# Performance work log

Hardware: AMD Instinct MI355X
Metric: run time of the kernel (lower is better)

## Reference

```python
import jax, jax.numpy as jnp
import numpy as np

B, S, D, H = 1, 2048, 768, 12
HD = D // H


def layer_norm(x, g, b, eps=1e-5):
    mu = x.mean(-1, keepdims=True)
    var = ((x - mu) ** 2).mean(-1, keepdims=True)
    return (x - mu) * jax.lax.rsqrt(var + eps) * g + b


def setup_inputs() -> dict:
    key = jax.random.key(0)
    ks = jax.random.split(key, 16)
    s = 0.02
    exp_encodings = jax.random.normal(ks[0], (B, S, D), dtype=jnp.float32)
    pert_encodings = jax.random.normal(ks[1], (B, S, D), dtype=jnp.float32)
    adj = (jax.random.uniform(ks[2], (S, S)) < 0.01).astype(jnp.int32)
    adj = adj.at[jnp.arange(S), jnp.arange(S)].set(1)
    in_proj_w = jax.random.normal(ks[3], (3 * D, D)) * s
    in_proj_b = jnp.zeros((3 * D,), jnp.float32)
    out_proj_w = jax.random.normal(ks[4], (D, D)) * s
    out_proj_b = jnp.zeros((D,), jnp.float32)
    ln0_g = jnp.ones((D,), jnp.float32); ln0_b = jnp.zeros((D,), jnp.float32)
    ln1_g = jnp.ones((D,), jnp.float32); ln1_b = jnp.zeros((D,), jnp.float32)
    ln2_g = jnp.ones((D,), jnp.float32); ln2_b = jnp.zeros((D,), jnp.float32)
    w1 = jax.random.normal(ks[5], (D // 2, D)) * s
    b1 = jnp.zeros((D // 2,), jnp.float32)
    w2 = jax.random.normal(ks[6], (D, D // 2)) * s
    b2 = jnp.zeros((D,), jnp.float32)
    return dict(exp_encodings=exp_encodings, pert_encodings=pert_encodings,
                in_proj_w=in_proj_w, in_proj_b=in_proj_b,
                out_proj_w=out_proj_w, out_proj_b=out_proj_b,
                ln0_g=ln0_g, ln0_b=ln0_b, ln1_g=ln1_g, ln1_b=ln1_b,
                ln2_g=ln2_g, ln2_b=ln2_b, w1=w1, b1=b1, w2=w2, b2=b2,
                adj=adj)


def reference(exp_encodings, pert_encodings, in_proj_w, in_proj_b,
              out_proj_w, out_proj_b, ln0_g, ln0_b, ln1_g, ln1_b,
              ln2_g, ln2_b, w1, b1, w2, b2, adj):
    b, s, d = exp_encodings.shape
    hd = d // H
    # additive mask: 0 where edge, -inf elsewhere (diag guaranteed edge)
    mask = jnp.where(adj > 0, 0.0, -jnp.inf).astype(exp_encodings.dtype)
    x_in = layer_norm(exp_encodings + pert_encodings, ln0_g, ln0_b)
    # torch MultiheadAttention (batch_first) self-attention
    qkv = x_in @ in_proj_w.T + in_proj_b          # [b,s,3d]
    q, k, v = jnp.split(qkv, 3, axis=-1)
    q = q.reshape(b, s, H, hd)
    k = k.reshape(b, s, H, hd)
    v = v.reshape(b, s, H, hd)
    scores = jnp.einsum('bqhe,bkhe->bhqk', q, k) / np.sqrt(hd) + mask
    attn = jax.nn.softmax(scores, axis=-1)
    o = jnp.einsum('bhqk,bkhe->bqhe', attn, v).reshape(b, s, d)
    o = o @ out_proj_w.T + out_proj_b
    x = layer_norm(o + x_in, ln1_g, ln1_b)
    ff = jax.nn.relu(x @ w1.T + b1) @ w2.T + b2
    return layer_norm(x + ff, ln2_g, ln2_b)
```

## Files before the change

kernel.cpp:

```cpp
#include <hip/hip_runtime.h>

#define S 2048
#define D 768
#define NH 12
#define HD 64
#define TD (3 * D)

typedef __bf16 bf16_t;
typedef __bf16 v8bf __attribute__((ext_vector_type(8)));
typedef __bf16 v4bf __attribute__((ext_vector_type(4)));
typedef float v4f __attribute__((ext_vector_type(4)));

__device__ __forceinline__ float wave_reduce_sum(float v) {
#pragma unroll
    for (int o = 32; o > 0; o >>= 1) v += __shfl_down(v, o, 64);
    return v;
}
__device__ float block_reduce_sum(float v) {
    __shared__ float t4[4];
    int lane = threadIdx.x & 63, wid = threadIdx.x >> 6;
    v = wave_reduce_sum(v);
    __syncthreads();
    if (lane == 0) t4[wid] = v;
    __syncthreads();
    return t4[0] + t4[1] + t4[2] + t4[3];
}

#define NW0 (TD * D / 4)
#define NW1 (D * D / 4)
#define NW2 ((D / 2) * D / 4)
#define NW3 (D * (D / 2) / 4)
#define NWALL (NW0 + NW1 + NW2 + NW3)

__global__ __launch_bounds__(256) void addln_cvt(const float* __restrict__ A, const float* __restrict__ Bv,
                                                 const float* __restrict__ g, const float* __restrict__ be,
                                                 bf16_t* __restrict__ out,
                                                 const float* __restrict__ s0, const float* __restrict__ s1,
                                                 const float* __restrict__ s2, const float* __restrict__ s3,
                                                 bf16_t* __restrict__ d0, bf16_t* __restrict__ d1,
                                                 bf16_t* __restrict__ d2, bf16_t* __restrict__ d3) {
    int blk = blockIdx.x, t = threadIdx.x;
    if (blk >= S) {
        int i = (blk - S) * 256 + t;
        const float* sp; bf16_t* dp;
        if (i < NW0) { sp = s0; dp = d0; }
        else if (i < NW0 + NW1) { sp = s1; dp = d1; i -= NW0; }
        else if (i < NW0 + NW1 + NW2) { sp = s2; dp = d2; i -= NW0 + NW1; }
        else if (i < NWALL) { sp = s3; dp = d3; i -= NW0 + NW1 + NW2; }
        else return;
        float4 v = ((const float4*)sp)[i];
        v4bf o = {(bf16_t)v.x, (bf16_t)v.y, (bf16_t)v.z, (bf16_t)v.w};
        *(v4bf*)(dp + (size_t)i * 4) = o;
        return;
    }
    int row = blk;
    const float* a = A + (size_t)row * D;
    const float* b = Bv + (size_t)row * D;
    float x[3];
    float s = 0.f;
#pragma unroll
    for (int i = 0; i < 3; ++i) { int c = t + 256 * i; x[i] = a[c] + b[c]; s += x[i]; }
    float mean = block_reduce_sum(s) * (1.0f / D);
    float vs = 0.f;
#pragma unroll
    for (int i = 0; i < 3; ++i) { float d = x[i] - mean; vs += d * d; }
    float var = block_reduce_sum(vs) * (1.0f / D);
    float rstd = rsqrtf(var + 1e-5f);
#pragma unroll
    for (int i = 0; i < 3; ++i) {
        int c = t + 256 * i;
        out[(size_t)row * D + c] = (bf16_t)((x[i] - mean) * rstd * g[c] + be[c]);
    }
}

template <typename TO>
__global__ __launch_bounds__(256) void ln_only(const bf16_t* __restrict__ X,
                                               const float* __restrict__ g, const float* __restrict__ be,
                                               TO* __restrict__ out) {
    int row = blockIdx.x, t = threadIdx.x;
    const bf16_t* a = X + (size_t)row * D;
    float x[3];
    float s = 0.f;
#pragma unroll
    for (int i = 0; i < 3; ++i) { int c = t + 256 * i; x[i] = (float)a[c]; s += x[i]; }
    float mean = block_reduce_sum(s) * (1.0f / D);
    float vs = 0.f;
#pragma unroll
    for (int i = 0; i < 3; ++i) { float d = x[i] - mean; vs += d * d; }
    float var = block_reduce_sum(vs) * (1.0f / D);
    float rstd = rsqrtf(var + 1e-5f);
#pragma unroll
    for (int i = 0; i < 3; ++i) {
        int c = t + 256 * i;
        out[(size_t)row * D + c] = (TO)((x[i] - mean) * rstd * g[c] + be[c]);
    }
}

#define GBK 64

template <int TM, int TN, int RELU, bool RESID>
__global__ __launch_bounds__(256) void gemm_mfma(const bf16_t* __restrict__ A, const bf16_t* __restrict__ B,
                                                 const float* __restrict__ bias,
                                                 const bf16_t* __restrict__ Rsd, bf16_t* __restrict__ C,
                                                 int M, int N, int K) {
    constexpr int CA = TM * 8;
    constexpr int CHUNKS = (TM + TN) * 8;
    constexpr int P = CHUNKS / 256;
    static_assert(CHUNKS % 256 == 0, "chunk passes must be exact");
    constexpr int MI = TM / 32, NI = TN / 32;
    __shared__ bf16_t As[TM * GBK];
    __shared__ bf16_t Bs[TN * GBK];
    const int t = threadIdx.x;
    const int lane = t & 63, wave = t >> 6;
    const int wr = (wave >> 1) * (TM / 2), wc = (wave & 1) * (TN / 2);
    const int m0 = blockIdx.y * TM, n0 = blockIdx.x * TN;
    const int lm = lane & 15, q = lane >> 4;

    const bf16_t* gsrc[P];
    bf16_t* ldst[P];
#pragma unroll
    for (int p = 0; p < P; ++p) {
        int c = t + 256 * p;
        if (c < CA) {
            int slab = c / (TM * 4), r4 = c % (TM * 4);
            int row = r4 >> 2, c4 = r4 & 3;
            gsrc[p] = A + (size_t)(m0 + row) * K + slab * 32 + c4 * 8;
            ldst[p] = As + slab * (TM * 32) + row * 32 + c4 * 8;
        } else {
            int cc = c - CA;
            int slab = cc / (TN * 4), r4 = cc % (TN * 4);
            int row = r4 >> 2, c4 = r4 & 3;
            gsrc[p] = B + (size_t)(n0 + row) * K + slab * 32 + c4 * 8;
            ldst[p] = Bs + slab * (TN * 32) + row * 32 + c4 * 8;
        }
    }

    v4f acc[MI][NI] = {};

    for (int k0 = 0; k0 < K; k0 += GBK) {
#pragma unroll
        for (int p = 0; p < P; ++p)
            __builtin_amdgcn_global_load_lds((const __attribute__((address_space(1))) void*)(gsrc[p] + k0),
                                             (__attribute__((address_space(3))) void*)ldst[p], 16, 0, 0);
        __syncthreads();

        v8bf af[2][MI], bfr[2][NI];
#pragma unroll
        for (int s = 0; s < 2; ++s) {
#pragma unroll
            for (int i = 0; i < MI; ++i)
                af[s][i] = *(const v8bf*)(As + s * (TM * 32) + (wr + i * 16 + lm) * 32 + q * 8);
#pragma unroll
            for (int j = 0; j < NI; ++j)
                bfr[s][j] = *(const v8bf*)(Bs + s * (TN * 32) + (wc + j * 16 + lm) * 32 + q * 8);
        }
#pragma unroll
        for (int s = 0; s < 2; ++s)
#pragma unroll
            for (int i = 0; i < MI; ++i)
#pragma unroll
                for (int j = 0; j < NI; ++j)
                    acc[i][j] = __builtin_amdgcn_mfma_f32_16x16x32_bf16(af[s][i], bfr[s][j], acc[i][j], 0, 0, 0);
        __syncthreads();
    }

#pragma unroll
    for (int i = 0; i < MI; ++i)
#pragma unroll
        for (int j = 0; j < NI; ++j) {
            int col = n0 + wc + j * 16 + lm;
            float bs = bias[col];
#pragma unroll
            for (int r = 0; r < 4; ++r) {
                int row = m0 + wr + i * 16 + q * 4 + r;
                float v = acc[i][j][r] + bs;
                if (RELU) v = fmaxf(v, 0.f);
                if (RESID) v += (float)Rsd[(size_t)row * N + col];
                C[(size_t)row * N + col] = (bf16_t)v;
            }
        }
}

#define FTM 32
#define FTN 64
#define FK  768
#define FN  384

__global__ __launch_bounds__(256) void ff1_ln_gemm(const bf16_t* __restrict__ y1,
                                                   const float* __restrict__ g, const float* __restrict__ be,
                                                   const bf16_t* __restrict__ B, const float* __restrict__ bias,
                                                   bf16_t* __restrict__ x1g, bf16_t* __restrict__ Cffh) {
    __shared__ bf16_t x1s[24 * 32 * 32];
    __shared__ bf16_t Bs[FTN * GBK];
    const int t = threadIdx.x, lane = t & 63, wave = t >> 6;
    const int m0 = blockIdx.y * FTM, n0 = blockIdx.x * FTN;
    const int lm = lane & 15, q = lane >> 4;

#pragma unroll
    for (int rr = 0; rr < 8; ++rr) {
        int row = wave * 8 + rr;
        const bf16_t* yp = y1 + (size_t)(m0 + row) * D;
        float v[12];
        float s = 0.f, s2 = 0.f;
#pragma unroll
        for (int e = 0; e < 12; ++e) {
            v[e] = (float)yp[lane + 64 * e];
            s += v[e]; s2 += v[e] * v[e];
        }
#pragma unroll
        for (int o = 32; o > 0; o >>= 1) { s += __shfl_xor(s, o, 64); s2 += __shfl_xor(s2, o, 64); }
        float mean = s * (1.0f / D);
        float var = s2 * (1.0f / D) - mean * mean;
        float rstd = rsqrtf(var + 1e-5f);
#pragma unroll
        for (int e = 0; e < 12; ++e) {
            int c = lane + 64 * e;
            bf16_t xv = (bf16_t)((v[e] - mean) * rstd * g[c] + be[c]);
            x1s[(c >> 5) * 1024 + row * 32 + (c & 31)] = xv;
            if (blockIdx.x == 0) x1g[(size_t)(m0 + row) * D + c] = xv;
        }
    }
    __syncthreads();

    const bf16_t* gsrc[2];
    bf16_t* ldst[2];
#pragma unroll
    for (int p = 0; p < 2; ++p) {
        int c = t + 256 * p;
        int slab = c >> 8, r4 = c & 255;
        int row = r4 >> 2, c4 = r4 & 3;
        gsrc[p] = B + (size_t)(n0 + row) * FK + slab * 32 + c4 * 8;
        ldst[p] = Bs + slab * (FTN * 32) + row * 32 + c4 * 8;
    }

    v4f acc[2] = {};
    const int wr = (wave >> 1) * 16, wc = (wave & 1) * 32;

    for (int k0 = 0; k0 < FK; k0 += GBK) {
#pragma unroll
        for (int p = 0; p < 2; ++p)
            __builtin_amdgcn_global_load_lds((const __attribute__((address_space(1))) void*)(gsrc[p] + k0),
                                             (__attribute__((address_space(3))) void*)ldst[p], 16, 0, 0);
        __syncthreads();

        v8bf af[2], bfr[2][2];
#pragma unroll
        for (int s = 0; s < 2; ++s) {
            af[s] = *(const v8bf*)(x1s + ((k0 >> 5) + s) * 1024 + (wr + lm) * 32 + q * 8);
#pragma unroll
            for (int j = 0; j < 2; ++j)
                bfr[s][j] = *(const v8bf*)(Bs + s * (FTN * 32) + (wc + j * 16 + lm) * 32 + q * 8);
        }
#pragma unroll
        for (int s = 0; s < 2; ++s)
#pragma unroll
            for (int j = 0; j < 2; ++j)
                acc[j] = __builtin_amdgcn_mfma_f32_16x16x32_bf16(af[s], bfr[s][j], acc[j], 0, 0, 0);
        __syncthreads();
    }

#pragma unroll
    for (int j = 0; j < 2; ++j) {
        int col = n0 + wc + j * 16 + lm;
        float bs = bias[col];
#pragma unroll
        for (int r = 0; r < 4; ++r) {
            int row = m0 + wr + q * 4 + r;
            Cffh[(size_t)row * FN + col] = (bf16_t)fmaxf(acc[j][r] + bs, 0.f);
        }
    }
}

__global__ __launch_bounds__(256) void attn_sparse(const bf16_t* __restrict__ qkv, const int* __restrict__ adj,
                                                   bf16_t* __restrict__ O) {
    __shared__ int s_idx[128];
    __shared__ int s_cnt;
    __shared__ float s_q[D];
    __shared__ float s_p[NH][128];

    const int row = blockIdx.x, t = threadIdx.x;
    const int lane = t & 63, wave = t >> 6;
    if (t == 0) s_cnt = 0;
    __syncthreads();

    const int4* arow = (const int4*)(adj + (size_t)row * S);
#pragma unroll
    for (int p = 0; p < 2; ++p) {
        int4 v = arow[t + 256 * p];
        int base = (t + 256 * p) * 4;
        if (v.x) { int k = atomicAdd(&s_cnt, 1); if (k < 128) s_idx[k] = base + 0; }
        if (v.y) { int k = atomicAdd(&s_cnt, 1); if (k < 128) s_idx[k] = base + 1; }
        if (v.z) { int k = atomicAdd(&s_cnt, 1); if (k < 128) s_idx[k] = base + 2; }
        if (v.w) { int k = atomicAdd(&s_cnt, 1); if (k < 128) s_idx[k] = base + 3; }
    }
    for (int c = t; c < D; c += 256) s_q[c] = (float)qkv[(size_t)row * TD + c];
    __syncthreads();
    const int n = (s_cnt < 128) ? s_cnt : 128;

    for (int it = t; it < n * NH; it += 256) {
        int h = it / n, i = it - h * n;
        int j = s_idx[i];
        const v8bf* kp = (const v8bf*)(qkv + (size_t)j * TD + D + h * HD);
        const float4* qp = (const float4*)(s_q + h * HD);
        float dot = 0.f;
#pragma unroll
        for (int c = 0; c < 8; ++c) {
            v8bf kv = kp[c];
            float4 qa = qp[2 * c], qb = qp[2 * c + 1];
            dot += qa.x * (float)kv[0] + qa.y * (float)kv[1] + qa.z * (float)kv[2] + qa.w * (float)kv[3]
                 + qb.x * (float)kv[4] + qb.y * (float)kv[5] + qb.z * (float)kv[6] + qb.w * (float)kv[7];
        }
        s_p[h][i] = dot * 0.125f;
    }
    __syncthreads();

    for (int h = wave; h < NH; h += 4) {
        float v0 = (lane < n) ? s_p[h][lane] : -1e30f;
        float v1 = (lane + 64 < n) ? s_p[h][lane + 64] : -1e30f;
        float m = fmaxf(v0, v1);
#pragma unroll
        for (int o = 32; o > 0; o >>= 1) m = fmaxf(m, __shfl_xor(m, o, 64));
        float p0 = (lane < n) ? __expf(v0 - m) : 0.f;
        float p1 = (lane + 64 < n) ? __expf(v1 - m) : 0.f;
        float sm = p0 + p1;
#pragma unroll
        for (int o = 32; o > 0; o >>= 1) sm += __shfl_xor(sm, o, 64);
        float inv = 1.f / sm;
        if (lane < n) s_p[h][lane] = p0 * inv;
        if (lane + 64 < n) s_p[h][lane + 64] = p1 * inv;
    }
    __syncthreads();

    for (int o = t; o < D; o += 256) {
        int h = o >> 6, e = o & 63;
        const float* pp = s_p[h];
        const bf16_t* vbase = qkv + 2 * D + h * HD + e;
        float a0 = 0.f, a1 = 0.f, a2 = 0.f, a3 = 0.f;
        int i = 0;
        for (; i + 4 <= n; i += 4) {
            int j0 = s_idx[i], j1 = s_idx[i + 1], j2 = s_idx[i + 2], j3 = s_idx[i + 3];
            a0 += pp[i]     * (float)vbase[(size_t)j0 * TD];
            a1 += pp[i + 1] * (float)vbase[(size_t)j1 * TD];
            a2 += pp[i + 2] * (float)vbase[(size_t)j2 * TD];
            a3 += pp[i + 3] * (float)vbase[(size_t)j3 * TD];
        }
        for (; i < n; ++i) a0 += pp[i] * (float)vbase[(size_t)s_idx[i] * TD];
        O[(size_t)row * D + o] = (bf16_t)((a0 + a1) + (a2 + a3));
    }
}

extern "C" void kernel_launch(void* const* d_in, const int* in_sizes, int n_in,
                              void* d_out, int out_size, void* d_ws, size_t ws_size,
                              hipStream_t stream) {
    const float* exp_e = (const float*)d_in[0];
    const float* pert  = (const float*)d_in[1];
    const float* w_in  = (const float*)d_in[2];
    const float* b_in  = (const float*)d_in[3];
    const float* w_out = (const float*)d_in[4];
    const float* b_out = (const float*)d_in[5];
    const float* g0  = (const float*)d_in[6];
    const float* be0 = (const float*)d_in[7];
    const float* g1  = (const float*)d_in[8];
    const float* be1 = (const float*)d_in[9];
    const float* g2  = (const float*)d_in[10];
    const float* be2 = (const float*)d_in[11];
    const float* w1  = (const float*)d_in[12];
    const float* b1  = (const float*)d_in[13];
    const float* w2  = (const float*)d_in[14];
    const float* b2  = (const float*)d_in[15];
    const int*   adj = (const int*)d_in[16];
    float* out = (float*)d_out;

    const size_t SD = (size_t)S * D;
    bf16_t* wb_in  = (bf16_t*)d_ws;
    bf16_t* wb_out = wb_in + (size_t)TD * D;
    bf16_t* wb_1   = wb_out + (size_t)D * D;
    bf16_t* wb_2   = wb_1 + (size_t)(D / 2) * D;
    bf16_t* x_in   = wb_2 + (size_t)D * (D / 2);
    bf16_t* qkv    = x_in + SD;
    bf16_t* attn_o = qkv + 3 * SD;
    bf16_t* y1     = attn_o + SD;
    bf16_t* x1     = y1 + SD;
    bf16_t* ffh    = x1 + SD;
    bf16_t* y2     = ffh + SD / 2;

    const int CVTB = (NWALL + 255) / 256;
    addln_cvt<<<S + CVTB, 256, 0, stream>>>(exp_e, pert, g0, be0, x_in,
                                            w_in, w_out, w1, w2, wb_in, wb_out, wb_1, wb_2);
    gemm_mfma<64, 128, 0, false><<<dim3(TD / 128, S / 64), 256, 0, stream>>>(x_in, wb_in, b_in, nullptr, qkv, S, TD, D);
    attn_sparse<<<S, 256, 0, stream>>>(qkv, adj, attn_o);
    gemm_mfma<64, 64, 0, true><<<dim3(D / 64, S / 64), 256, 0, stream>>>(attn_o, wb_out, b_out, x_in, y1, S, D, D);
    ff1_ln_gemm<<<dim3(FN / FTN, S / FTM), 256, 0, stream>>>(y1, g1, be1, wb_1, b1, x1, ffh);
    gemm_mfma<64, 64, 0, true><<<dim3(D / 64, S / 64), 256, 0, stream>>>(ffh, wb_2, b2, x1, y2, S, D, D / 2);
    ln_only<float><<<S, 256, 0, stream>>>(y2, g2, be2, out);
}
```

Baseline: 203.6 us.

## Fuse out-proj, LN1, FFN and LN2 into one per-row-block tail kernel

```diff
diff --git a/kernel.cpp b/kernel.cpp
--- a/kernel.cpp
+++ b/kernel.cpp
@@ -73,35 +73,11 @@
     }
 }
 
-template <typename TO>
-__global__ __launch_bounds__(256) void ln_only(const bf16_t* __restrict__ X,
-                                               const float* __restrict__ g, const float* __restrict__ be,
-                                               TO* __restrict__ out) {
-    int row = blockIdx.x, t = threadIdx.x;
-    const bf16_t* a = X + (size_t)row * D;
-    float x[3];
-    float s = 0.f;
-#pragma unroll
-    for (int i = 0; i < 3; ++i) { int c = t + 256 * i; x[i] = (float)a[c]; s += x[i]; }
-    float mean = block_reduce_sum(s) * (1.0f / D);
-    float vs = 0.f;
-#pragma unroll
-    for (int i = 0; i < 3; ++i) { float d = x[i] - mean; vs += d * d; }
-    float var = block_reduce_sum(vs) * (1.0f / D);
-    float rstd = rsqrtf(var + 1e-5f);
-#pragma unroll
-    for (int i = 0; i < 3; ++i) {
-        int c = t + 256 * i;
-        out[(size_t)row * D + c] = (TO)((x[i] - mean) * rstd * g[c] + be[c]);
-    }
-}
-
 #define GBK 64
 
-template <int TM, int TN, int RELU, bool RESID>
+template <int TM, int TN>
 __global__ __launch_bounds__(256) void gemm_mfma(const bf16_t* __restrict__ A, const bf16_t* __restrict__ B,
-                                                 const float* __restrict__ bias,
-                                                 const bf16_t* __restrict__ Rsd, bf16_t* __restrict__ C,
+                                                 const float* __restrict__ bias, bf16_t* __restrict__ C,
                                                  int M, int N, int K) {
     constexpr int CA = TM * 8;
     constexpr int CHUNKS = (TM + TN) * 8;
@@ -173,102 +149,9 @@
 #pragma unroll
             for (int r = 0; r < 4; ++r) {
                 int row = m0 + wr + i * 16 + q * 4 + r;
-                float v = acc[i][j][r] + bs;
-                if (RELU) v = fmaxf(v, 0.f);
-                if (RESID) v += (float)Rsd[(size_t)row * N + col];
-                C[(size_t)row * N + col] = (bf16_t)v;
+                C[(size_t)row * N + col] = (bf16_t)(acc[i][j][r] + bs);
             }
         }
-}
-
-#define FTM 32
-#define FTN 64
-#define FK  768
-#define FN  384
-
-__global__ __launch_bounds__(256) void ff1_ln_gemm(const bf16_t* __restrict__ y1,
-                                                   const float* __restrict__ g, const float* __restrict__ be,
-                                                   const bf16_t* __restrict__ B, const float* __restrict__ bias,
-                                                   bf16_t* __restrict__ x1g, bf16_t* __restrict__ Cffh) {
-    __shared__ bf16_t x1s[24 * 32 * 32];
-    __shared__ bf16_t Bs[FTN * GBK];
-    const int t = threadIdx.x, lane = t & 63, wave = t >> 6;
-    const int m0 = blockIdx.y * FTM, n0 = blockIdx.x * FTN;
-    const int lm = lane & 15, q = lane >> 4;
-
-#pragma unroll
-    for (int rr = 0; rr < 8; ++rr) {
-        int row = wave * 8 + rr;
-        const bf16_t* yp = y1 + (size_t)(m0 + row) * D;
-        float v[12];
-        float s = 0.f, s2 = 0.f;
-#pragma unroll
-        for (int e = 0; e < 12; ++e) {
-            v[e] = (float)yp[lane + 64 * e];
-            s += v[e]; s2 += v[e] * v[e];
-        }
-#pragma unroll
-        for (int o = 32; o > 0; o >>= 1) { s += __shfl_xor(s, o, 64); s2 += __shfl_xor(s2, o, 64); }
-        float mean = s * (1.0f / D);
-        float var = s2 * (1.0f / D) - mean * mean;
-        float rstd = rsqrtf(var + 1e-5f);
-#pragma unroll
-        for (int e = 0; e < 12; ++e) {
-            int c = lane + 64 * e;
-            bf16_t xv = (bf16_t)((v[e] - mean) * rstd * g[c] + be[c]);
-            x1s[(c >> 5) * 1024 + row * 32 + (c & 31)] = xv;
-            if (blockIdx.x == 0) x1g[(size_t)(m0 + row) * D + c] = xv;
-        }
-    }
-    __syncthreads();
-
-    const bf16_t* gsrc[2];
-    bf16_t* ldst[2];
-#pragma unroll
-    for (int p = 0; p < 2; ++p) {
-        int c = t + 256 * p;
-        int slab = c >> 8, r4 = c & 255;
-        int row = r4 >> 2, c4 = r4 & 3;
-        gsrc[p] = B + (size_t)(n0 + row) * FK + slab * 32 + c4 * 8;
-        ldst[p] = Bs + slab * (FTN * 32) + row * 32 + c4 * 8;
-    }
-
-    v4f acc[2] = {};
-    const int wr = (wave >> 1) * 16, wc = (wave & 1) * 32;
-
-    for (int k0 = 0; k0 < FK; k0 += GBK) {
-#pragma unroll
-        for (int p = 0; p < 2; ++p)
-            __builtin_amdgcn_global_load_lds((const __attribute__((address_space(1))) void*)(gsrc[p] + k0),
-                                             (__attribute__((address_space(3))) void*)ldst[p], 16, 0, 0);
-        __syncthreads();
-
-        v8bf af[2], bfr[2][2];
-#pragma unroll
-        for (int s = 0; s < 2; ++s) {
-            af[s] = *(const v8bf*)(x1s + ((k0 >> 5) + s) * 1024 + (wr + lm) * 32 + q * 8);
-#pragma unroll
-            for (int j = 0; j < 2; ++j)
-                bfr[s][j] = *(const v8bf*)(Bs + s * (FTN * 32) + (wc + j * 16 + lm) * 32 + q * 8);
-        }
-#pragma unroll
-        for (int s = 0; s < 2; ++s)
-#pragma unroll
-            for (int j = 0; j < 2; ++j)
-                acc[j] = __builtin_amdgcn_mfma_f32_16x16x32_bf16(af[s], bfr[s][j], acc[j], 0, 0, 0);
-        __syncthreads();
-    }
-
-#pragma unroll
-    for (int j = 0; j < 2; ++j) {
-        int col = n0 + wc + j * 16 + lm;
-        float bs = bias[col];
-#pragma unroll
-        for (int r = 0; r < 4; ++r) {
-            int row = m0 + wr + q * 4 + r;
-            Cffh[(size_t)row * FN + col] = (bf16_t)fmaxf(acc[j][r] + bs, 0.f);
-        }
-    }
 }
 
 __global__ __launch_bounds__(256) void attn_sparse(const bf16_t* __restrict__ qkv, const int* __restrict__ adj,
@@ -346,6 +229,174 @@
         }
         for (; i < n; ++i) a0 += pp[i] * (float)vbase[(size_t)s_idx[i] * TD];
         O[(size_t)row * D + o] = (bf16_t)((a0 + a1) + (a2 + a3));
+    }
+}
+
+#define RB 8
+
+__global__ __launch_bounds__(256) void tail_fused(
+    const bf16_t* __restrict__ attn_o, const bf16_t* __restrict__ x_in,
+    const bf16_t* __restrict__ wo, const float* __restrict__ bo,
+    const float* __restrict__ g1, const float* __restrict__ be1,
+    const bf16_t* __restrict__ w1, const float* __restrict__ b1,
+    const bf16_t* __restrict__ w2, const float* __restrict__ b2,
+    const float* __restrict__ g2, const float* __restrict__ be2,
+    float* __restrict__ out) {
+    __shared__ bf16_t Afrag[24 * 16 * 32];
+    __shared__ bf16_t Scr[RB * D];
+    __shared__ bf16_t Ybuf[RB * D];
+    const int t = threadIdx.x, lane = t & 63, wave = t >> 6;
+    const int lm = lane & 15, q = lane >> 4;
+    const int m0 = blockIdx.x * RB;
+
+    {
+        int row = t >> 5, cc = t & 31;
+#pragma unroll
+        for (int i = 0; i < 3; ++i) {
+            int c0 = (cc + 32 * i) * 8;
+            *(v8bf*)(Afrag + (c0 >> 5) * 512 + row * 32 + (c0 & 31)) =
+                *(const v8bf*)(attn_o + (size_t)(m0 + row) * D + c0);
+            *(v8bf*)(Scr + row * D + c0) =
+                *(const v8bf*)(x_in + (size_t)(m0 + row) * D + c0);
+        }
+    }
+    __syncthreads();
+
+#pragma unroll 1
+    for (int g = 0; g < 4; ++g) {
+        const int ct0 = wave * 12 + g * 3;
+        v4f a0 = {}, a1 = {}, a2 = {};
+        const bf16_t* b0p = wo + (size_t)(ct0 * 16 + lm) * D + q * 8;
+        const bf16_t* b1p = b0p + (size_t)16 * D;
+        const bf16_t* b2p = b0p + (size_t)32 * D;
+        const bf16_t* ap = Afrag + lm * 32 + q * 8;
+#pragma unroll 4
+        for (int k = 0; k < 24; ++k) {
+            v8bf a = *(const v8bf*)(ap + k * 512);
+            a0 = __builtin_amdgcn_mfma_f32_16x16x32_bf16(a, *(const v8bf*)(b0p + k * 32), a0, 0, 0, 0);
+            a1 = __builtin_amdgcn_mfma_f32_16x16x32_bf16(a, *(const v8bf*)(b1p + k * 32), a1, 0, 0, 0);
+            a2 = __builtin_amdgcn_mfma_f32_16x16x32_bf16(a, *(const v8bf*)(b2p + k * 32), a2, 0, 0, 0);
+        }
+        if (q < 2) {
+            v4f ac[3] = {a0, a1, a2};
+#pragma unroll
+            for (int j = 0; j < 3; ++j) {
+                int col = (ct0 + j) * 16 + lm;
+                float bb = bo[col];
+#pragma unroll
+                for (int r = 0; r < 4; ++r) {
+                    int row = q * 4 + r;
+                    Ybuf[row * D + col] = (bf16_t)(ac[j][r] + bb + (float)Scr[row * D + col]);
+                }
+            }
+        }
+    }
+    __syncthreads();
+
+#pragma unroll 1
+    for (int rr = 0; rr < 2; ++rr) {
+        const int row = wave * 2 + rr;
+        float v[12];
+        float s = 0.f, s2 = 0.f;
+#pragma unroll
+        for (int e = 0; e < 12; ++e) {
+            v[e] = (float)Ybuf[row * D + lane + 64 * e];
+            s += v[e]; s2 += v[e] * v[e];
+        }
+#pragma unroll
+        for (int o = 32; o > 0; o >>= 1) { s += __shfl_xor(s, o, 64); s2 += __shfl_xor(s2, o, 64); }
+        float mean = s * (1.0f / D);
+        float rstd = rsqrtf(s2 * (1.0f / D) - mean * mean + 1e-5f);
+#pragma unroll
+        for (int e = 0; e < 12; ++e) {
+            int c = lane + 64 * e;
+            Afrag[(c >> 5) * 512 + row * 32 + (c & 31)] = (bf16_t)((v[e] - mean) * rstd * g1[c] + be1[c]);
+        }
+    }
+    __syncthreads();
+
+#pragma unroll 1
+    for (int g = 0; g < 2; ++g) {
+        const int ct0 = wave * 6 + g * 3;
+        v4f a0 = {}, a1 = {}, a2 = {};
+        const bf16_t* b0p = w1 + (size_t)(ct0 * 16 + lm) * D + q * 8;
+        const bf16_t* b1p = b0p + (size_t)16 * D;
+        const bf16_t* b2p = b0p + (size_t)32 * D;
+        const bf16_t* ap = Afrag + lm * 32 + q * 8;
+#pragma unroll 4
+        for (int k = 0; k < 24; ++k) {
+            v8bf a = *(const v8bf*)(ap + k * 512);
+            a0 = __builtin_amdgcn_mfma_f32_16x16x32_bf16(a, *(const v8bf*)(b0p + k * 32), a0, 0, 0, 0);
+            a1 = __builtin_amdgcn_mfma_f32_16x16x32_bf16(a, *(const v8bf*)(b1p + k * 32), a1, 0, 0, 0);
+            a2 = __builtin_amdgcn_mfma_f32_16x16x32_bf16(a, *(const v8bf*)(b2p + k * 32), a2, 0, 0, 0);
+        }
+        if (q < 2) {
+            v4f ac[3] = {a0, a1, a2};
+#pragma unroll
+            for (int j = 0; j < 3; ++j) {
+                int col = (ct0 + j) * 16 + lm;
+                float bb = b1[col];
+#pragma unroll
+                for (int r = 0; r < 4; ++r) {
+                    int row = q * 4 + r;
+                    Scr[(col >> 5) * 512 + row * 32 + (col & 31)] = (bf16_t)fmaxf(ac[j][r] + bb, 0.f);
+                }
+            }
+        }
+    }
+    __syncthreads();
+
+#pragma unroll 1
+    for (int g = 0; g < 4; ++g) {
+        const int ct0 = wave * 12 + g * 3;
+        v4f a0 = {}, a1 = {}, a2 = {};
+        const bf16_t* b0p = w2 + (size_t)(ct0 * 16 + lm) * 384 + q * 8;
+        const bf16_t* b1p = b0p + (size_t)16 * 384;
+        const bf16_t* b2p = b0p + (size_t)32 * 384;
+        const bf16_t* ap = Scr + lm * 32 + q * 8;
+#pragma unroll
+        for (int k = 0; k < 12; ++k) {
+            v8bf a = *(const v8bf*)(ap + k * 512);
+            a0 = __builtin_amdgcn_mfma_f32_16x16x32_bf16(a, *(const v8bf*)(b0p + k * 32), a0, 0, 0, 0);
+            a1 = __builtin_amdgcn_mfma_f32_16x16x32_bf16(a, *(const v8bf*)(b1p + k * 32), a1, 0, 0, 0);
+            a2 = __builtin_amdgcn_mfma_f32_16x16x32_bf16(a, *(const v8bf*)(b2p + k * 32), a2, 0, 0, 0);
+        }
+        if (q < 2) {
+            v4f ac[3] = {a0, a1, a2};
+#pragma unroll
+            for (int j = 0; j < 3; ++j) {
+                int col = (ct0 + j) * 16 + lm;
+                float bb = b2[col];
+#pragma unroll
+                for (int r = 0; r < 4; ++r) {
+                    int row = q * 4 + r;
+                    float x1v = (float)Afrag[(col >> 5) * 512 + row * 32 + (col & 31)];
+                    Ybuf[row * D + col] = (bf16_t)(ac[j][r] + bb + x1v);
+                }
+            }
+        }
+    }
+    __syncthreads();
+
+#pragma unroll 1
+    for (int rr = 0; rr < 2; ++rr) {
+        const int row = wave * 2 + rr;
+        float v[12];
+        float s = 0.f, s2 = 0.f;
+#pragma unroll
+        for (int e = 0; e < 12; ++e) {
+            v[e] = (float)Ybuf[row * D + lane + 64 * e];
+            s += v[e]; s2 += v[e] * v[e];
+        }
+#pragma unroll
+        for (int o = 32; o > 0; o >>= 1) { s += __shfl_xor(s, o, 64); s2 += __shfl_xor(s2, o, 64); }
+        float mean = s * (1.0f / D);
+        float rstd = rsqrtf(s2 * (1.0f / D) - mean * mean + 1e-5f);
+#pragma unroll
+        for (int e = 0; e < 12; ++e) {
+            int c = lane + 64 * e;
+            out[(size_t)(m0 + row) * D + c] = (v[e] - mean) * rstd * g2[c] + be2[c];
+        }
     }
 }
 
@@ -379,18 +430,12 @@
     bf16_t* x_in   = wb_2 + (size_t)D * (D / 2);
     bf16_t* qkv    = x_in + SD;
     bf16_t* attn_o = qkv + 3 * SD;
-    bf16_t* y1     = attn_o + SD;
-    bf16_t* x1     = y1 + SD;
-    bf16_t* ffh    = x1 + SD;
-    bf16_t* y2     = ffh + SD / 2;
 
     const int CVTB = (NWALL + 255) / 256;
     addln_cvt<<<S + CVTB, 256, 0, stream>>>(exp_e, pert, g0, be0, x_in,
                                             w_in, w_out, w1, w2, wb_in, wb_out, wb_1, wb_2);
-    gemm_mfma<64, 128, 0, false><<<dim3(TD / 128, S / 64), 256, 0, stream>>>(x_in, wb_in, b_in, nullptr, qkv, S, TD, D);
+    gemm_mfma<64, 128><<<dim3(TD / 128, S / 64), 256, 0, stream>>>(x_in, wb_in, b_in, qkv, S, TD, D);
     attn_sparse<<<S, 256, 0, stream>>>(qkv, adj, attn_o);
-    gemm_mfma<64, 64, 0, true><<<dim3(D / 64, S / 64), 256, 0, stream>>>(attn_o, wb_out, b_out, x_in, y1, S, D, D);
-    ff1_ln_gemm<<<dim3(FN / FTN, S / FTM), 256, 0, stream>>>(y1, g1, be1, wb_1, b1, x1, ffh);
-    gemm_mfma<64, 64, 0, true><<<dim3(D / 64, S / 64), 256, 0, stream>>>(ffh, wb_2, b2, x1, y2, S, D, D / 2);
-    ln_only<float><<<S, 256, 0, stream>>>(y2, g2, be2, out);
-}
+    tail_fused<<<S / RB, 256, 0, stream>>>(attn_o, x_in, wb_out, b_out, g1, be1,
+                                           wb_1, b1, wb_2, b2, g2, be2, out);
+}
```

Result: slower. 234.4 us (+15.1%).
